# Optimization experiments

Hardware: AMD Instinct MI355X
Metric: run time of the kernel (lower is better)

## Reference

```python
import jax, jax.numpy as jnp
import numpy as np

# ---- static configuration (from init_kwargs) ----
K = 2                 # kernel_size -> (2K+1)^2 = 25 window offsets
WIN = 2 * K + 1       # 5
A = WIN * WIN         # 25 window slots (ir_in replicated A times)
MUL_IN = 16           # multiplicity of each input irrep (16x0e + 16x1e)
MUL_OUT = 32          # 32x0e + 32x1e
SH0 = float(1.0 / (2.0 * np.sqrt(np.pi)))       # Y_l=0, e3nn 'integral' norm
SH1 = float(np.sqrt(3.0 / (4.0 * np.pi)))       # Y_l=1 scale (normalize=False)
CG_110 = float(1.0 / np.sqrt(3.0))              # CG for 1x1 -> 0 (dot/sqrt3)
CG_111 = float(1.0 / np.sqrt(2.0))              # CG for 1x1 -> 1 (cross/sqrt2)
# path normalization: out irrep gets 1/sqrt(fan_in) with fan = n_paths * mul_u
A0 = float(1.0 / np.sqrt(2 * A * MUL_IN))       # 0e fed by paths (0e,0e)+(1e,1e) per slot
A1 = float(1.0 / np.sqrt(3 * A * MUL_IN))       # 1e fed by (0e,1e)+(1e,0e)+(1e,1e)


def setup_inputs() -> dict:
    key = jax.random.key(0)
    ks = jax.random.split(key, 7)
    feat = jax.random.normal(ks[0], (8, 64, 64, 64), dtype=jnp.float32)
    spin = jax.random.normal(ks[1], (8, 64, 64, 3), dtype=jnp.float32)
    wshape = (A, MUL_IN, MUL_OUT)  # one uvw block per window slot per path type
    W_000 = jax.random.normal(ks[2], wshape, dtype=jnp.float32)
    W_110 = jax.random.normal(ks[3], wshape, dtype=jnp.float32)
    W_011 = jax.random.normal(ks[4], wshape, dtype=jnp.float32)
    W_101 = jax.random.normal(ks[5], wshape, dtype=jnp.float32)
    W_111 = jax.random.normal(ks[6], wshape, dtype=jnp.float32)
    return {"feat": feat, "spin": spin, "W_000": W_000, "W_110": W_110,
            "W_011": W_011, "W_101": W_101, "W_111": W_111}


def spin2colsq2d(feat):
    # circular im2col: (N,Lx,Ly,F) -> (N,Lx,Ly,A,F)
    N, Lx, Ly, F = feat.shape
    p = jnp.pad(feat, ((0, 0), (K, K), (K, K), (0, 0)), mode='wrap')
    cols = [p[:, ix:ix + Lx, iy:iy + Ly, :]
            for ix in range(WIN) for iy in range(WIN)]
    return jnp.stack(cols, axis=3)


def reference(feat, spin, W_000, W_110, W_011, W_101, W_111):
    col = spin2colsq2d(feat)                                  # (N,Lx,Ly,A,64)
    x0 = col[..., :MUL_IN]                                    # (N,Lx,Ly,A,16) scalars
    x1 = col[..., MUL_IN:].reshape(col.shape[:-1] + (MUL_IN, 3))  # (N,Lx,Ly,A,16,3)
    # spherical harmonics of spin, l=0..1, normalize=False, integral norm
    sh1 = SH1 * spin                                          # (N,Lx,Ly,3)
    # ---- paths into 0e output ----
    dot = jnp.einsum('nxyaui,nxyi->nxyau', x1, sh1) * CG_110  # 1e x 1e -> 0e
    out0 = A0 * (SH0 * jnp.einsum('nxyau,auw->nxyw', x0, W_000)
                 + jnp.einsum('nxyau,auw->nxyw', dot, W_110))  # (N,Lx,Ly,32)
    # ---- paths into 1e output ----
    cross = jnp.cross(x1, sh1[..., None, None, :]) * CG_111   # 1e x 1e -> 1e
    out1 = A1 * (jnp.einsum('nxyau,nxyi,auw->nxywi', x0, sh1, W_011)
                 + SH0 * jnp.einsum('nxyaui,auw->nxywi', x1, W_101)
                 + jnp.einsum('nxyaui,auw->nxywi', cross, W_111))  # (N,Lx,Ly,32,3)
    out1 = out1.reshape(out1.shape[:-2] + (MUL_OUT * 3,))
    return jnp.concatenate([out0, out1], axis=-1)             # (N,Lx,Ly,128)
```

## Files before the change

### kernel.cpp

```cpp
#include <hip/hip_runtime.h>


typedef __attribute__((ext_vector_type(8))) short short8;
typedef __attribute__((ext_vector_type(16))) float f32x16;
typedef __attribute__((ext_vector_type(4))) float float4v;

typedef __attribute__((address_space(3))) unsigned char lds_u8_t;
typedef const __attribute__((address_space(1))) unsigned char g_u8_t;

#define FEATT_BYTES (8u * 64u * 64u * 64u * 2u)
#define BT_OFFSET   FEATT_BYTES

#define MFMA32(A, B, C) __builtin_amdgcn_mfma_f32_32x32x16_bf16(A, B, C, 0, 0, 0)

__device__ __forceinline__ unsigned short f2bf(float f) {
    unsigned int u = __float_as_uint(f);
    return (unsigned short)((u + 0x7FFFu + ((u >> 16) & 1u)) >> 16);
}

__global__ __launch_bounds__(256) void prep_kernel(
    const float* __restrict__ feat,
    const float* __restrict__ W000, const float* __restrict__ W110,
    const float* __restrict__ W011, const float* __restrict__ W101,
    const float* __restrict__ W111,
    unsigned char* __restrict__ ws)
{
    int tid = threadIdx.x;
    int b = blockIdx.x;
    if (b < 512) {
        __shared__ float sf[64][68];
        size_t base = (size_t)b * 4096;
        #pragma unroll
        for (int i = 0; i < 4; ++i) {
            int e = tid + i * 256;
            float4v v = *(const float4v*)(feat + base + (size_t)e * 4);
            int px = e >> 4;
            int c  = (e & 15) * 4;
            sf[px][c + 0] = v[0]; sf[px][c + 1] = v[1];
            sf[px][c + 2] = v[2]; sf[px][c + 3] = v[3];
        }
        __syncthreads();
        unsigned short* dst = (unsigned short*)ws + base;
        #pragma unroll
        for (int i = 0; i < 2; ++i) {
            int t = tid + i * 256;
            int s = t >> 6, px = t & 63;
            short8 o;
            #pragma unroll
            for (int j = 0; j < 8; ++j) {
                int chp = s * 8 + j;
                int c = (chp < 16) ? chp : (16 + 3 * ((chp - 16) & 15) + ((chp - 16) >> 4));
                o[j] = (short)f2bf(sf[px][c]);
            }
            *(short8*)(dst + s * 512 + px * 8) = o;
        }
    } else {
        int t = (b - 512) * 256 + tid;
        if (t >= 4000) return;
        int a = t / 160, colv = t - a * 160;
        int arr = colv >> 5, w = colv & 31;
        const float* Wp = (arr == 0) ? W000 : (arr == 1) ? W011
                        : (arr == 2) ? W110 : (arr == 3) ? W101 : W111;
        unsigned short tmp[16];
        #pragma unroll
        for (int k = 0; k < 16; ++k) tmp[k] = f2bf(Wp[a * 512 + k * 32 + w]);
        unsigned short* d = (unsigned short*)(ws + BT_OFFSET) + (size_t)t * 16;
        *(short8*)(d)     = *(short8*)(tmp);
        *(short8*)(d + 8) = *(short8*)(tmp + 8);
    }
}

__global__ __launch_bounds__(256, 2) void spinconv_mfma_kernel(
    const unsigned char* __restrict__ featT8,
    const unsigned char* __restrict__ bt,
    const float* __restrict__ spin,
    float* __restrict__ out)
{
    const float SH0f   = 0.28209479177387814f;
    const float CG110f = 0.5773502691896258f;
    const float CG111f = 0.7071067811865476f;
    const float A0f    = 0.035355339059327376f;
    const float A1f    = 0.028867513459481287f;

    __shared__ __align__(16) unsigned char fl[5 * 8 * 64 * 16];
    __shared__ float s_lds[192];

    int tid = threadIdx.x;
    int b = blockIdx.x;
    int bid = ((b & 7) << 6) + (b >> 3);
    int x = bid & 63;

    int lane = tid & 63;
    int wv4 = tid >> 6;

    #pragma unroll
    for (int i = 0; i < 10; ++i) {
        int g = wv4 * 10 + i;
        int dx = g >> 3;
        int X = (x + dx + 62) & 63;
        const unsigned char* src = featT8
            + (size_t)(bid - x + X) * 8192 + (g & 7) * 1024 + lane * 16;
        __builtin_amdgcn_global_load_lds((g_u8_t*)src, (lds_u8_t*)(fl + g * 1024), 16, 0, 0);
    }
    if (tid < 192) {
        s_lds[tid] = 0.4886025119029199f * spin[(size_t)bid * 192 + tid];
    }
    __syncthreads();

    int pair = wv4 >> 1;
    int role = (wv4 & 1) ^ (bid & 1);
    int col = lane & 31;
    int khalf = lane >> 5;
    int yb = pair << 5;
    int p0 = bid << 6;

    const unsigned char* bbase = bt + col * 32 + khalf * 16;
    float* rowbuf = (float*)fl;

    f32x16 zz;
    #pragma unroll
    for (int i = 0; i < 16; ++i) zz[i] = 0.f;

    f32x16 ac0 = zz, ac1 = zz, ac2 = zz, ac3 = zz, ac4 = zz, ac5 = zz;

    if (role == 0) {
        short8 B0c, B1c, B2c, B3c, B4c, B0n, B1n, B2n, B3n, B4n;
        short8 Axc, C0c, Axn, C0n;

        auto loadB = [&](int a, short8& b0, short8& b1, short8& b2, short8& b3, short8& b4) {
            const unsigned char* p = bbase + a * 5120;
            b0 = *(const short8*)(p);
            b1 = *(const short8*)(p + 1024);
            b2 = *(const short8*)(p + 2048);
            b3 = *(const short8*)(p + 3072);
            b4 = *(const short8*)(p + 4096);
        };
        auto loadA = [&](int a, short8& ax, short8& c0) {
            int ix = a / 5;
            int iy = a - ix * 5;
            int yn = (yb + col + iy + 62) & 63;
            const unsigned char* ab = fl + ix * 8192 + yn * 16;
            ax = *(const short8*)(ab + (0 + khalf) * 1024);
            c0 = *(const short8*)(ab + (2 + khalf) * 1024);
        };

        loadB(0, B0c, B1c, B2c, B3c, B4c);
        loadA(0, Axc, C0c);
        #pragma unroll
        for (int ap = 0; ap < 25; ap += 2) {
            if (ap + 1 < 25) { loadB(ap + 1, B0n, B1n, B2n, B3n, B4n); loadA(ap + 1, Axn, C0n); }
            __builtin_amdgcn_s_setprio(1);
            ac0 = MFMA32(Axc, B0c, ac0);
            ac1 = MFMA32(Axc, B1c, ac1);
            ac2 = MFMA32(C0c, B2c, ac2);
            ac3 = MFMA32(C0c, B3c, ac3);
            ac4 = MFMA32(C0c, B4c, ac4);
            __builtin_amdgcn_s_setprio(0);
            if (ap + 1 < 25) {
                if (ap + 2 < 25) { loadB(ap + 2, B0c, B1c, B2c, B3c, B4c); loadA(ap + 2, Axc, C0c); }
                __builtin_amdgcn_s_setprio(1);
                ac0 = MFMA32(Axn, B0n, ac0);
                ac1 = MFMA32(Axn, B1n, ac1);
                ac2 = MFMA32(C0n, B2n, ac2);
                ac3 = MFMA32(C0n, B3n, ac3);
                ac4 = MFMA32(C0n, B4n, ac4);
                __builtin_amdgcn_s_setprio(0);
            }
        }
    } else {
        short8 B2c, B3c, B4c, B2n, B3n, B4n;
        short8 C1c, C2c, C1n, C2n;

        auto loadB = [&](int a, short8& b2, short8& b3, short8& b4) {
            const unsigned char* p = bbase + a * 5120;
            b2 = *(const short8*)(p + 2048);
            b3 = *(const short8*)(p + 3072);
            b4 = *(const short8*)(p + 4096);
        };
        auto loadA = [&](int a, short8& c1, short8& c2) {
            int ix = a / 5;
            int iy = a - ix * 5;
            int yn = (yb + col + iy + 62) & 63;
            const unsigned char* ab = fl + ix * 8192 + yn * 16;
            c1 = *(const short8*)(ab + (4 + khalf) * 1024);
            c2 = *(const short8*)(ab + (6 + khalf) * 1024);
        };

        loadB(0, B2c, B3c, B4c);
        loadA(0, C1c, C2c);
        #pragma unroll
        for (int ap = 0; ap < 25; ap += 2) {
            if (ap + 1 < 25) { loadB(ap + 1, B2n, B3n, B4n); loadA(ap + 1, C1n, C2n); }
            __builtin_amdgcn_s_setprio(1);
            ac0 = MFMA32(C1c, B2c, ac0);
            ac1 = MFMA32(C2c, B2c, ac1);
            ac2 = MFMA32(C1c, B3c, ac2);
            ac3 = MFMA32(C2c, B3c, ac3);
            ac4 = MFMA32(C1c, B4c, ac4);
            ac5 = MFMA32(C2c, B4c, ac5);
            __builtin_amdgcn_s_setprio(0);
            if (ap + 1 < 25) {
                if (ap + 2 < 25) { loadB(ap + 2, B2c, B3c, B4c); loadA(ap + 2, C1c, C2c); }
                __builtin_amdgcn_s_setprio(1);
                ac0 = MFMA32(C1n, B2n, ac0);
                ac1 = MFMA32(C2n, B2n, ac1);
                ac2 = MFMA32(C1n, B3n, ac2);
                ac3 = MFMA32(C2n, B3n, ac3);
                ac4 = MFMA32(C1n, B4n, ac4);
                ac5 = MFMA32(C2n, B4n, ac5);
                __builtin_amdgcn_s_setprio(0);
            }
        }
    }

    __syncthreads();

    if (role == 0) {
        #pragma unroll
        for (int r = 0; r < 16; ++r) {
            int row = (r & 3) + ((r >> 2) << 3) + (khalf << 2);
            int y = yb + row;
            float s0 = s_lds[y * 3 + 0];
            float s1 = s_lds[y * 3 + 1];
            float s2 = s_lds[y * 3 + 2];
            float S000 = ac0[r], S011 = ac1[r];
            float V0 = ac2[r], T0 = ac3[r], U0 = ac4[r];
            rowbuf[y * 128 + col] = A0f * (SH0f * S000 + CG110f * s0 * V0);
            float* rp = rowbuf + y * 128 + 32 + 3 * col;
            rp[0] = A1f * (s0 * S011 + SH0f * T0);
            rp[1] = A1f * (s1 * S011 - CG111f * U0 * s2);
            rp[2] = A1f * (s2 * S011 + CG111f * U0 * s1);
        }
    }
    __syncthreads();
    if (role == 1) {
        #pragma unroll
        for (int r = 0; r < 16; ++r) {
            int row = (r & 3) + ((r >> 2) << 3) + (khalf << 2);
            int y = yb + row;
            float s0 = s_lds[y * 3 + 0];
            float s1 = s_lds[y * 3 + 1];
            float s2 = s_lds[y * 3 + 2];
            float V1 = ac0[r], V2 = ac1[r];
            float T1 = ac2[r], T2 = ac3[r];
            float U1 = ac4[r], U2 = ac5[r];
            rowbuf[y * 128 + col] += A0f * CG110f * (s1 * V1 + s2 * V2);
            float* rp = rowbuf + y * 128 + 32 + 3 * col;
            rp[0] += A1f * CG111f * (U1 * s2 - U2 * s1);
            rp[1] += A1f * (SH0f * T1 + CG111f * U2 * s0);
            rp[2] += A1f * (SH0f * T2 - CG111f * U1 * s0);
        }
    }
    __syncthreads();

    float* ob = out + (size_t)p0 * 128;
    #pragma unroll
    for (int i = 0; i < 8; ++i) {
        int e = (tid + (i << 8)) << 2;
        *(float4v*)(ob + e) = *(const float4v*)(rowbuf + e);
    }
}

extern "C" void kernel_launch(void* const* d_in, const int* in_sizes, int n_in,
                              void* d_out, int out_size, void* d_ws, size_t ws_size,
                              hipStream_t stream) {
    const float* feat = (const float*)d_in[0];
    const float* spin = (const float*)d_in[1];
    const float* W000 = (const float*)d_in[2];
    const float* W110 = (const float*)d_in[3];
    const float* W011 = (const float*)d_in[4];
    const float* W101 = (const float*)d_in[5];
    const float* W111 = (const float*)d_in[6];
    float* out = (float*)d_out;
    unsigned char* ws = (unsigned char*)d_ws;

    hipLaunchKernelGGL(prep_kernel, dim3(528), dim3(256), 0, stream,
                       feat, W000, W110, W011, W101, W111, ws);
    hipLaunchKernelGGL(spinconv_mfma_kernel, dim3(512), dim3(256), 0, stream,
                       ws, ws + BT_OFFSET, spin, out);
}
```

Measured before the change: 24.80 us.

## Split MFMA work across eight waves with four balanced path roles

```diff
diff --git a/kernel.cpp b/kernel.cpp
--- a/kernel.cpp
+++ b/kernel.cpp
@@ -70,7 +70,7 @@
     }
 }
 
-__global__ __launch_bounds__(256, 2) void spinconv_mfma_kernel(
+__global__ __launch_bounds__(512, 4) void spinconv_mfma_kernel(
     const unsigned char* __restrict__ featT8,
     const unsigned char* __restrict__ bt,
     const float* __restrict__ spin,
@@ -91,11 +91,11 @@
     int x = bid & 63;
 
     int lane = tid & 63;
-    int wv4 = tid >> 6;
-
-    #pragma unroll
-    for (int i = 0; i < 10; ++i) {
-        int g = wv4 * 10 + i;
+    int wv8 = tid >> 6;
+
+    #pragma unroll
+    for (int i = 0; i < 5; ++i) {
+        int g = wv8 * 5 + i;
         int dx = g >> 3;
         int X = (x + dx + 62) & 63;
         const unsigned char* src = featT8
@@ -107,8 +107,8 @@
     }
     __syncthreads();
 
-    int pair = wv4 >> 1;
-    int role = (wv4 & 1) ^ (bid & 1);
+    int pair = wv8 >> 2;
+    int role = (wv8 + pair) & 3;
     int col = lane & 31;
     int khalf = lane >> 5;
     int yb = pair << 5;
@@ -121,142 +121,115 @@
     #pragma unroll
     for (int i = 0; i < 16; ++i) zz[i] = 0.f;
 
-    f32x16 ac0 = zz, ac1 = zz, ac2 = zz, ac3 = zz, ac4 = zz, ac5 = zz;
+    f32x16 ac0 = zz, ac1 = zz, ac2 = zz;
 
     if (role == 0) {
-        short8 B0c, B1c, B2c, B3c, B4c, B0n, B1n, B2n, B3n, B4n;
-        short8 Axc, C0c, Axn, C0n;
-
-        auto loadB = [&](int a, short8& b0, short8& b1, short8& b2, short8& b3, short8& b4) {
+        short8 B0c, B1c, B0n, B1n, Axc, Axn;
+        auto loadB = [&](int a, short8& b0, short8& b1) {
             const unsigned char* p = bbase + a * 5120;
             b0 = *(const short8*)(p);
             b1 = *(const short8*)(p + 1024);
-            b2 = *(const short8*)(p + 2048);
-            b3 = *(const short8*)(p + 3072);
-            b4 = *(const short8*)(p + 4096);
-        };
-        auto loadA = [&](int a, short8& ax, short8& c0) {
+        };
+        auto loadA = [&](int a, short8& ax) {
+            int ix = a / 5;
+            int iy = a - ix * 5;
+            int yn = (yb + col + iy + 62) & 63;
+            ax = *(const short8*)(fl + ix * 8192 + yn * 16 + khalf * 1024);
+        };
+        loadB(0, B0c, B1c);
+        loadA(0, Axc);
+        #pragma unroll
+        for (int ap = 0; ap < 25; ap += 2) {
+            if (ap + 1 < 25) { loadB(ap + 1, B0n, B1n); loadA(ap + 1, Axn); }
+            __builtin_amdgcn_s_setprio(1);
+            ac0 = MFMA32(Axc, B0c, ac0);
+            ac1 = MFMA32(Axc, B1c, ac1);
+            __builtin_amdgcn_s_setprio(0);
+            if (ap + 1 < 25) {
+                if (ap + 2 < 25) { loadB(ap + 2, B0c, B1c); loadA(ap + 2, Axc); }
+                __builtin_amdgcn_s_setprio(1);
+                ac0 = MFMA32(Axn, B0n, ac0);
+                ac1 = MFMA32(Axn, B1n, ac1);
+                __builtin_amdgcn_s_setprio(0);
+            }
+        }
+    } else {
+        const int matoff = (role + 1) << 10;
+        short8 Bc, Bn, C0c, C1c, C2c, C0n, C1n, C2n;
+        auto loadB = [&](int a, short8& bb) {
+            bb = *(const short8*)(bbase + a * 5120 + matoff);
+        };
+        auto loadA = [&](int a, short8& c0, short8& c1, short8& c2) {
             int ix = a / 5;
             int iy = a - ix * 5;
             int yn = (yb + col + iy + 62) & 63;
             const unsigned char* ab = fl + ix * 8192 + yn * 16;
-            ax = *(const short8*)(ab + (0 + khalf) * 1024);
             c0 = *(const short8*)(ab + (2 + khalf) * 1024);
-        };
-
-        loadB(0, B0c, B1c, B2c, B3c, B4c);
-        loadA(0, Axc, C0c);
+            c1 = *(const short8*)(ab + (4 + khalf) * 1024);
+            c2 = *(const short8*)(ab + (6 + khalf) * 1024);
+        };
+        loadB(0, Bc);
+        loadA(0, C0c, C1c, C2c);
         #pragma unroll
         for (int ap = 0; ap < 25; ap += 2) {
-            if (ap + 1 < 25) { loadB(ap + 1, B0n, B1n, B2n, B3n, B4n); loadA(ap + 1, Axn, C0n); }
+            if (ap + 1 < 25) { loadB(ap + 1, Bn); loadA(ap + 1, C0n, C1n, C2n); }
             __builtin_amdgcn_s_setprio(1);
-            ac0 = MFMA32(Axc, B0c, ac0);
-            ac1 = MFMA32(Axc, B1c, ac1);
-            ac2 = MFMA32(C0c, B2c, ac2);
-            ac3 = MFMA32(C0c, B3c, ac3);
-            ac4 = MFMA32(C0c, B4c, ac4);
+            ac0 = MFMA32(C0c, Bc, ac0);
+            ac1 = MFMA32(C1c, Bc, ac1);
+            ac2 = MFMA32(C2c, Bc, ac2);
             __builtin_amdgcn_s_setprio(0);
             if (ap + 1 < 25) {
-                if (ap + 2 < 25) { loadB(ap + 2, B0c, B1c, B2c, B3c, B4c); loadA(ap + 2, Axc, C0c); }
+                if (ap + 2 < 25) { loadB(ap + 2, Bc); loadA(ap + 2, C0c, C1c, C2c); }
                 __builtin_amdgcn_s_setprio(1);
-                ac0 = MFMA32(Axn, B0n, ac0);
-                ac1 = MFMA32(Axn, B1n, ac1);
-                ac2 = MFMA32(C0n, B2n, ac2);
-                ac3 = MFMA32(C0n, B3n, ac3);
-                ac4 = MFMA32(C0n, B4n, ac4);
+                ac0 = MFMA32(C0n, Bn, ac0);
+                ac1 = MFMA32(C1n, Bn, ac1);
+                ac2 = MFMA32(C2n, Bn, ac2);
                 __builtin_amdgcn_s_setprio(0);
             }
         }
-    } else {
-        short8 B2c, B3c, B4c, B2n, B3n, B4n;
-        short8 C1c, C2c, C1n, C2n;
-
-        auto loadB = [&](int a, short8& b2, short8& b3, short8& b4) {
-            const unsigned char* p = bbase + a * 5120;
-            b2 = *(const short8*)(p + 2048);
-            b3 = *(const short8*)(p + 3072);
-            b4 = *(const short8*)(p + 4096);
-        };
-        auto loadA = [&](int a, short8& c1, short8& c2) {
-            int ix = a / 5;
-            int iy = a - ix * 5;
-            int yn = (yb + col + iy + 62) & 63;
-            const unsigned char* ab = fl + ix * 8192 + yn * 16;
-            c1 = *(const short8*)(ab + (4 + khalf) * 1024);
-            c2 = *(const short8*)(ab + (6 + khalf) * 1024);
-        };
-
-        loadB(0, B2c, B3c, B4c);
-        loadA(0, C1c, C2c);
-        #pragma unroll
-        for (int ap = 0; ap < 25; ap += 2) {
-            if (ap + 1 < 25) { loadB(ap + 1, B2n, B3n, B4n); loadA(ap + 1, C1n, C2n); }
-            __builtin_amdgcn_s_setprio(1);
-            ac0 = MFMA32(C1c, B2c, ac0);
-            ac1 = MFMA32(C2c, B2c, ac1);
-            ac2 = MFMA32(C1c, B3c, ac2);
-            ac3 = MFMA32(C2c, B3c, ac3);
-            ac4 = MFMA32(C1c, B4c, ac4);
-            ac5 = MFMA32(C2c, B4c, ac5);
-            __builtin_amdgcn_s_setprio(0);
-            if (ap + 1 < 25) {
-                if (ap + 2 < 25) { loadB(ap + 2, B2c, B3c, B4c); loadA(ap + 2, C1c, C2c); }
-                __builtin_amdgcn_s_setprio(1);
-                ac0 = MFMA32(C1n, B2n, ac0);
-                ac1 = MFMA32(C2n, B2n, ac1);
-                ac2 = MFMA32(C1n, B3n, ac2);
-                ac3 = MFMA32(C2n, B3n, ac3);
-                ac4 = MFMA32(C1n, B4n, ac4);
-                ac5 = MFMA32(C2n, B4n, ac5);
-                __builtin_amdgcn_s_setprio(0);
-            }
-        }
     }
 
     __syncthreads();
 
-    if (role == 0) {
-        #pragma unroll
-        for (int r = 0; r < 16; ++r) {
-            int row = (r & 3) + ((r >> 2) << 3) + (khalf << 2);
-            int y = yb + row;
-            float s0 = s_lds[y * 3 + 0];
-            float s1 = s_lds[y * 3 + 1];
-            float s2 = s_lds[y * 3 + 2];
-            float S000 = ac0[r], S011 = ac1[r];
-            float V0 = ac2[r], T0 = ac3[r], U0 = ac4[r];
-            rowbuf[y * 128 + col] = A0f * (SH0f * S000 + CG110f * s0 * V0);
-            float* rp = rowbuf + y * 128 + 32 + 3 * col;
-            rp[0] = A1f * (s0 * S011 + SH0f * T0);
-            rp[1] = A1f * (s1 * S011 - CG111f * U0 * s2);
-            rp[2] = A1f * (s2 * S011 + CG111f * U0 * s1);
-        }
-    }
-    __syncthreads();
-    if (role == 1) {
-        #pragma unroll
-        for (int r = 0; r < 16; ++r) {
-            int row = (r & 3) + ((r >> 2) << 3) + (khalf << 2);
-            int y = yb + row;
-            float s0 = s_lds[y * 3 + 0];
-            float s1 = s_lds[y * 3 + 1];
-            float s2 = s_lds[y * 3 + 2];
-            float V1 = ac0[r], V2 = ac1[r];
-            float T1 = ac2[r], T2 = ac3[r];
-            float U1 = ac4[r], U2 = ac5[r];
-            rowbuf[y * 128 + col] += A0f * CG110f * (s1 * V1 + s2 * V2);
-            float* rp = rowbuf + y * 128 + 32 + 3 * col;
-            rp[0] += A1f * CG111f * (U1 * s2 - U2 * s1);
-            rp[1] += A1f * (SH0f * T1 + CG111f * U2 * s0);
-            rp[2] += A1f * (SH0f * T2 - CG111f * U1 * s0);
-        }
-    }
-    __syncthreads();
+    #pragma unroll
+    for (int ph = 0; ph < 4; ++ph) {
+        if (role == ph) {
+            #pragma unroll
+            for (int r = 0; r < 16; ++r) {
+                int row = (r & 3) + ((r >> 2) << 3) + (khalf << 2);
+                int y = yb + row;
+                float s0 = s_lds[y * 3 + 0];
+                float s1 = s_lds[y * 3 + 1];
+                float s2 = s_lds[y * 3 + 2];
+                float* rb = rowbuf + y * 128;
+                float* rp = rb + 32 + 3 * col;
+                if (ph == 0) {
+                    float S000 = ac0[r], S011 = ac1[r];
+                    rb[col] = A0f * SH0f * S000;
+                    rp[0] = A1f * s0 * S011;
+                    rp[1] = A1f * s1 * S011;
+                    rp[2] = A1f * s2 * S011;
+                } else if (ph == 1) {
+                    rb[col] += A0f * CG110f * (s0 * ac0[r] + s1 * ac1[r] + s2 * ac2[r]);
+                } else if (ph == 2) {
+                    rp[0] += A1f * SH0f * ac0[r];
+                    rp[1] += A1f * SH0f * ac1[r];
+                    rp[2] += A1f * SH0f * ac2[r];
+                } else {
+                    float U0 = ac0[r], U1 = ac1[r], U2 = ac2[r];
+                    rp[0] += A1f * CG111f * (U1 * s2 - U2 * s1);
+                    rp[1] += A1f * CG111f * (U2 * s0 - U0 * s2);
+                    rp[2] += A1f * CG111f * (U0 * s1 - U1 * s0);
+                }
+            }
+        }
+        __syncthreads();
+    }
 
     float* ob = out + (size_t)p0 * 128;
     #pragma unroll
-    for (int i = 0; i < 8; ++i) {
-        int e = (tid + (i << 8)) << 2;
+    for (int i = 0; i < 4; ++i) {
+        int e = (tid + (i << 9)) << 2;
         *(float4v*)(ob + e) = *(const float4v*)(rowbuf + e);
     }
 }
@@ -276,6 +249,6 @@
 
     hipLaunchKernelGGL(prep_kernel, dim3(528), dim3(256), 0, stream,
                        feat, W000, W110, W011, W101, W111, ws);
-    hipLaunchKernelGGL(spinconv_mfma_kernel, dim3(512), dim3(256), 0, stream,
+    hipLaunchKernelGGL(spinconv_mfma_kernel, dim3(512), dim3(512), 0, stream,
                        ws, ws + BT_OFFSET, spin, out);
 }
```

New measurement: 24.78 us. Within noise of the previous version (-0.1%).
